# Optimization experiments

Measured on AMD Instinct MI355X. Metric: run time of the kernel, lower is better.

Reference implementation:

```python
import jax, jax.numpy as jnp
from jax import lax
import numpy as np


def conv2d(x, w, pad):
    # x: NCHW, w: OIHW
    return lax.conv_general_dilated(
        x, w, window_strides=(1, 1), padding=[(pad, pad), (pad, pad)],
        dimension_numbers=("NCHW", "OIHW", "NCHW"))


def _scan_dir(x, a, axis, reverse):
    """Directional IRNN scan: cur = relu(x_i + alpha * prev), prev0 = 0.
    a broadcasts as (1, C, 1) over the remaining (B, C, L) slice dims."""
    if reverse:
        x = jnp.flip(x, axis)
    xs = jnp.moveaxis(x, axis, 0)  # (L, B, C, other)

    def step(prev, xi):
        cur = jax.nn.relu(xi + a * prev)
        return cur, cur

    _, hs = lax.scan(step, jnp.zeros_like(xs[0]), xs)
    h = jnp.moveaxis(hs, 0, axis)
    if reverse:
        h = jnp.flip(h, axis)
    return h


def spatial_irnn(x, alpha):
    a = alpha.reshape(1, -1, 1)  # broadcasts over (B, C, W) or (B, C, H)
    h_td = _scan_dir(x, a, axis=2, reverse=False)  # top -> down
    h_dt = _scan_dir(x, a, axis=2, reverse=True)   # down -> top
    h_lr = _scan_dir(x, a, axis=3, reverse=False)  # left -> right
    h_rl = _scan_dir(x, a, axis=3, reverse=True)   # right -> left
    return h_td, h_lr, h_dt, h_rl


def setup_inputs() -> dict:
    key = jax.random.key(0)
    ks = jax.random.split(key, 10)
    B, C, H, W = 8, 32, 256, 256
    mid = C // 2
    s = 0.05
    return {
        "x": jax.random.normal(ks[0], (B, C, H, W), jnp.float32),
        "alpha1": jnp.full((C,), 0.2, jnp.float32),
        "alpha2": jnp.full((C,), 0.2, jnp.float32),
        "w_in": jax.random.normal(ks[1], (C, C, 3, 3), jnp.float32) * s,
        "w2": jax.random.normal(ks[2], (C, 4 * C, 3, 3), jnp.float32) * s,
        "w3": jax.random.normal(ks[3], (C, 4 * C, 3, 3), jnp.float32) * s,
        "att_w1": jax.random.normal(ks[4], (mid, C, 3, 3), jnp.float32) * s,
        "att_w2": jax.random.normal(ks[5], (mid, mid, 3, 3), jnp.float32) * s,
        "att_w3": jax.random.normal(ks[6], (4, mid, 1, 1), jnp.float32) * s,
        "att_b3": jnp.zeros((4,), jnp.float32),
        "w_out": jax.random.normal(ks[7], (1, C, 1, 1), jnp.float32) * s,
    }


def reference(x, alpha1, alpha2, w_in, w2, w3, att_w1, att_w2, att_w3, att_b3, w_out):
    # Attention gate: 4 per-direction weight maps in (0,1)
    a = jax.nn.relu(conv2d(x, att_w1, pad=1))
    a = jax.nn.relu(conv2d(a, att_w2, pad=1))
    weight = jax.nn.sigmoid(conv2d(a, att_w3, pad=0) + att_b3.reshape(1, -1, 1, 1))

    def gate(up, right, down, left):
        return jnp.concatenate([
            up * weight[:, 0:1], right * weight[:, 1:2],
            down * weight[:, 2:3], left * weight[:, 3:4]], axis=1)

    out = conv2d(x, w_in, pad=1)
    up, right, down, left = spatial_irnn(out, alpha1)
    out = conv2d(gate(up, right, down, left), w2, pad=1)
    up, right, down, left = spatial_irnn(out, alpha2)
    out = jax.nn.relu(conv2d(gate(up, right, down, left), w3, pad=1))
    mask = jax.nn.sigmoid(conv2d(out, w_out, pad=0))
    return mask
```

## Files before the change

kernel.cpp:

```cpp
#include <hip/hip_runtime.h>
#include <cstddef>

#define H_ 256
#define W_ 256
#define HW_ 65536

typedef unsigned int uint;
typedef unsigned short ushort;
typedef __attribute__((ext_vector_type(8))) short short8;
typedef __attribute__((ext_vector_type(16))) float floatx16;

__device__ __forceinline__ float bf2f(ushort u) {
    return __uint_as_float(((uint)u) << 16);
}
__device__ __forceinline__ ushort f2bf(float f) {
    uint u = __float_as_uint(f);
    uint r = (u + 0x7fffu + ((u >> 16) & 1u)) >> 16;
    return (ushort)r;
}
__device__ __forceinline__ float sigmoidf_(float x) {
    return 1.0f / (1.0f + expf(-x));
}

__device__ __forceinline__ void prep_one(const float* src, ushort* dst,
                                         int CO, int CI, int e) {
    int chunk = e / 9216;
    int r = e - chunk * 9216;
    int co = r / 288;
    int kk = r - co * 288;
    int khw = kk >> 5;
    int ci = kk & 31;
    int cig = chunk * 32 + ci;
    float v = 0.f;
    if (co < CO && cig < CI) v = src[(co * CI + cig) * 9 + khw];
    int s = kk >> 4;
    int lane = ((kk >> 3) & 1) * 32 + co;
    int j = kk & 7;
    dst[(((size_t)chunk * 18 + s) * 64 + lane) * 8 + j] = f2bf(v);
}

__global__ __launch_bounds__(256) void prep_weights(
    const float* __restrict__ w_in, const float* __restrict__ w2,
    const float* __restrict__ w3, const float* __restrict__ aw1,
    const float* __restrict__ aw2,
    ushort* __restrict__ w_inB, ushort* __restrict__ w2B,
    ushort* __restrict__ w3B, ushort* __restrict__ aw1B,
    ushort* __restrict__ aw2B) {
    int idx = blockIdx.x * 256 + threadIdx.x;
    if (idx < 9216)        prep_one(w_in, w_inB, 32, 32, idx);
    else if (idx < 46080)  prep_one(w2, w2B, 32, 128, idx - 9216);
    else if (idx < 82944)  prep_one(w3, w3B, 32, 128, idx - 46080);
    else if (idx < 92160)  prep_one(aw1, aw1B, 16, 32, idx - 82944);
    else if (idx < 101376) prep_one(aw2, aw2B, 16, 16, idx - 92160);
}

__global__ __launch_bounds__(256) void transform_x(const float* __restrict__ x,
                                                   ushort* __restrict__ xh) {
    __shared__ float s[64][33];
    const int t = threadIdx.x;
    const int w0 = blockIdx.x * 64, h = blockIdx.y, b = blockIdx.z;
    {
        int ww = t & 63, c0 = (t >> 6) * 8;
#pragma unroll
        for (int j = 0; j < 8; j++) {
            int c = c0 + j;
            s[ww][c] = x[((size_t)(b * 32 + c)) * HW_ + h * W_ + w0 + ww];
        }
    }
    __syncthreads();
    {
        int p = t >> 2, cb = t & 3;
        ushort tmp[8];
#pragma unroll
        for (int j = 0; j < 8; j++) tmp[j] = f2bf(s[p][cb * 8 + j]);
        *(uint4*)(xh + (((size_t)b * HW_ + h * W_ + w0 + p) * 32) + cb * 8) =
            *(const uint4*)tmp;
    }
}

template<int NCHUNK, int COOUT, bool RELU>
__global__ __launch_bounds__(256, 4) void conv_mfma(
    const ushort* __restrict__ in0, const ushort* __restrict__ in1,
    const ushort* __restrict__ in2, const ushort* __restrict__ in3,
    const ushort* __restrict__ wB, ushort* __restrict__ outp) {
    __shared__ __align__(16) ushort smem[1360 * 8];
    const int t = threadIdx.x;
    const int wid = t >> 6;
    const int lane = t & 63;
    const int lco = lane & 31, lhalf = lane >> 5;
    const int w0 = blockIdx.x * 32, h0 = blockIdx.y * 8, b = blockIdx.z;
    const ushort* ins[4] = {in0, in1, in2, in3};

    size_t goff[6];
    int slot[6];
    bool ok[6];
#pragma unroll
    for (int i = 0; i < 6; i++) {
        int u = i * 256 + t;
        int row = u / 136;
        int rem = u - row * 136;
        int p = rem >> 2, cb = rem & 3;
        int gh = h0 - 1 + row, gw = w0 - 1 + p;
        ok[i] = (u < 1360) && ((unsigned)gh < 256u) && ((unsigned)gw < 256u);
        goff[i] = ok[i] ? ((((size_t)b * HW_ + (size_t)gh * W_ + gw) * 32) + cb * 8) : 0;
        slot[i] = row * 136 + (p << 2) + (cb ^ (p & 3) ^ ((p >> 2) & 3));
    }

    floatx16 acc0, acc1;
#pragma unroll
    for (int i = 0; i < 16; i++) { acc0[i] = 0.f; acc1[i] = 0.f; }

    for (int ch = 0; ch < NCHUNK; ch++) {
        __syncthreads();
        {
            const ushort* inp = ins[ch];
            uint4 v[6];
#pragma unroll
            for (int i = 0; i < 6; i++) {
                v[i] = make_uint4(0, 0, 0, 0);
                if (ok[i]) v[i] = *(const uint4*)(inp + goff[i]);
            }
#pragma unroll
            for (int i = 0; i < 6; i++) {
                int u = i * 256 + t;
                if (u < 1360) *(uint4*)(smem + (size_t)slot[i] * 8) = v[i];
            }
        }
        __syncthreads();

        const ushort* wbp = wB + ((size_t)ch * 18 * 64 + lane) * 8;
#pragma unroll
        for (int half = 0; half < 2; half++) {
            short8 bf[9];
#pragma unroll
            for (int j = 0; j < 9; j++)
                bf[j] = *(const short8*)(wbp + (size_t)(2 * j + half) * 512);
            const int cbr = half * 2 + lhalf;
#pragma unroll
            for (int kw = 0; kw < 3; kw++) {
                const int ww = lco + kw;
                const int cbs = cbr ^ (ww & 3) ^ ((ww >> 2) & 3);
                short8 a[4];
#pragma unroll
                for (int r = 0; r < 4; r++)
                    a[r] = *(const short8*)(smem + (size_t)((wid * 2 + r) * 136 + (ww << 2) + cbs) * 8);
#pragma unroll
                for (int kh = 0; kh < 3; kh++) {
                    acc0 = __builtin_amdgcn_mfma_f32_32x32x16_bf16(a[kh], bf[kh * 3 + kw], acc0, 0, 0, 0);
                    acc1 = __builtin_amdgcn_mfma_f32_32x32x16_bf16(a[kh + 1], bf[kh * 3 + kw], acc1, 0, 0, 0);
                }
            }
        }
    }

#pragma unroll
    for (int r = 0; r < 16; r++) {
        int prow = (r & 3) + 8 * (r >> 2) + 4 * lhalf;
        float v0 = acc0[r], v1 = acc1[r];
        if (RELU) { v0 = fmaxf(v0, 0.f); v1 = fmaxf(v1, 0.f); }
        ushort u0 = (lco < COOUT) ? f2bf(v0) : (ushort)0;
        ushort u1 = (lco < COOUT) ? f2bf(v1) : (ushort)0;
        size_t p0 = (((size_t)b * HW_ + (h0 + wid * 2) * W_ + w0 + prow) * 32) + lco;
        outp[p0] = u0;
        outp[p0 + (size_t)W_ * 32] = u1;
    }
}

__global__ __launch_bounds__(256) void att1x1(const ushort* __restrict__ a2,
                                              const float* __restrict__ w,
                                              const float* __restrict__ bias,
                                              ushort* __restrict__ wmapT) {
    int idx = blockIdx.x * 256 + threadIdx.x;
    float xin[16];
    {
        uint4 v0 = *(const uint4*)(a2 + (size_t)idx * 32);
        uint4 v1 = *(const uint4*)(a2 + (size_t)idx * 32 + 8);
        const ushort* u = (const ushort*)&v0;
#pragma unroll
        for (int j = 0; j < 8; j++) xin[j] = bf2f(u[j]);
        const ushort* u2 = (const ushort*)&v1;
#pragma unroll
        for (int j = 0; j < 8; j++) xin[8 + j] = bf2f(u2[j]);
    }
#pragma unroll
    for (int g = 0; g < 4; g++) {
        float acc = bias[g];
#pragma unroll
        for (int ci = 0; ci < 16; ci++) acc = fmaf(xin[ci], w[g * 16 + ci], acc);
        wmapT[(size_t)g * 8 * HW_ + idx] = f2bf(sigmoidf_(acc));
    }
}

__global__ __launch_bounds__(256) void out1x1(const ushort* __restrict__ feat,
                                              const float* __restrict__ w,
                                              float* __restrict__ out) {
    int idx = blockIdx.x * 256 + threadIdx.x;
    float acc = 0.f;
    const ushort* f = feat + (size_t)idx * 32;
#pragma unroll
    for (int q = 0; q < 4; q++) {
        uint4 v = *(const uint4*)(f + q * 8);
        const ushort* u = (const ushort*)&v;
#pragma unroll
        for (int j = 0; j < 8; j++) acc = fmaf(bf2f(u[j]), w[q * 8 + j], acc);
    }
    out[idx] = sigmoidf_(acc);
}

template<int VERT>
__global__ __launch_bounds__(256) void scan_seg(
    const ushort* __restrict__ feat, const float* __restrict__ alpha,
    const ushort* __restrict__ wmapT, ushort* __restrict__ gfwd,
    ushort* __restrict__ gbwd, int gf, int gb) {
    const int t = threadIdx.x;
    const int cg = t & 3;
    const int bx = blockIdx.x;
    const int col = (bx & 3) * 64 + (t >> 2);
    const int seg = (bx >> 2) & 7;
    const int dir = (bx >> 5) & 1;
    const int b = bx >> 6;
    const int c0 = cg * 8;

    float a[8];
#pragma unroll
    for (int j = 0; j < 8; j++) a[j] = alpha[c0 + j];

    const ushort* wplane = wmapT + (size_t)(dir ? gb : gf) * 8 * HW_ + (size_t)b * HW_;
    ushort* gout = dir ? gbwd : gfwd;

    const int main0 = seg * 32;
    const int start = (seg == 0) ? 0 : main0 - 16;
    const int cnt = main0 - start + 32;

    auto pixof = [&](int p) -> size_t {
        int phys = dir ? 255 - p : p;
        return VERT ? ((size_t)phys * W_ + col) : ((size_t)col * W_ + phys);
    };

    uint4 xv[4];
    ushort wv[4];
#pragma unroll
    for (int k = 0; k < 4; k++) {
        size_t pix = pixof(start + k);
        xv[k] = *(const uint4*)(feat + ((size_t)b * HW_ + pix) * 32 + c0);
        wv[k] = wplane[pix];
    }
    float prev[8];
#pragma unroll
    for (int j = 0; j < 8; j++) prev[j] = 0.f;

    for (int i = 0; i < cnt; i += 4) {
#pragma unroll
        for (int k = 0; k < 4; k++) {
            const int p = start + i + k;
            uint4 xcur = xv[k];
            ushort wcur = wv[k];
            if (i + k + 4 < cnt) {
                size_t pix = pixof(p + 4);
                xv[k] = *(const uint4*)(feat + ((size_t)b * HW_ + pix) * 32 + c0);
                wv[k] = wplane[pix];
            }
            const ushort* xu = (const ushort*)&xcur;
            if (p >= main0) {
                float wmv = bf2f(wcur);
                ushort o[8];
#pragma unroll
                for (int j = 0; j < 8; j++) {
                    float cur = fmaxf(fmaf(a[j], prev[j], bf2f(xu[j])), 0.f);
                    prev[j] = cur;
                    o[j] = f2bf(cur * wmv);
                }
                *(uint4*)(gout + ((size_t)b * HW_ + pixof(p)) * 32 + c0) = *(const uint4*)o;
            } else {
#pragma unroll
                for (int j = 0; j < 8; j++)
                    prev[j] = fmaxf(fmaf(a[j], prev[j], bf2f(xu[j])), 0.f);
            }
        }
    }
}

extern "C" void kernel_launch(void* const* d_in, const int* in_sizes, int n_in,
                              void* d_out, int out_size, void* d_ws, size_t ws_size,
                              hipStream_t stream) {
    const float* x      = (const float*)d_in[0];
    const float* alpha1 = (const float*)d_in[1];
    const float* alpha2 = (const float*)d_in[2];
    const float* w_in   = (const float*)d_in[3];
    const float* w2     = (const float*)d_in[4];
    const float* w3     = (const float*)d_in[5];
    const float* aw1    = (const float*)d_in[6];
    const float* aw2    = (const float*)d_in[7];
    const float* aw3    = (const float*)d_in[8];
    const float* ab3    = (const float*)d_in[9];
    const float* wout   = (const float*)d_in[10];
    float* out = (float*)d_out;

    const size_t TEN = (size_t)8 * HW_ * 32;
    ushort* p = (ushort*)d_ws;
    ushort* xh    = p; p += TEN;
    ushort* feat  = p; p += TEN;
    ushort* g0    = p; p += TEN;
    ushort* g1    = p; p += TEN;
    ushort* g2    = p; p += TEN;
    ushort* g3    = p; p += TEN;
    ushort* wmapT = p; p += (size_t)4 * 8 * HW_;
    ushort* w_inB = p; p += 9216;
    ushort* w2B   = p; p += 36864;
    ushort* w3B   = p; p += 36864;
    ushort* aw1B  = p; p += 9216;
    ushort* aw2B  = p; p += 9216;

    prep_weights<<<396, 256, 0, stream>>>(w_in, w2, w3, aw1, aw2,
                                          w_inB, w2B, w3B, aw1B, aw2B);
    transform_x<<<dim3(4, 256, 8), 256, 0, stream>>>(x, xh);

    dim3 gconv(8, 32, 8);
    conv_mfma<1, 16, true><<<gconv, 256, 0, stream>>>(xh, xh, xh, xh, aw1B, g0);
    conv_mfma<1, 16, true><<<gconv, 256, 0, stream>>>(g0, g0, g0, g0, aw2B, g1);
    att1x1<<<2048, 256, 0, stream>>>(g1, aw3, ab3, wmapT);

    conv_mfma<1, 32, false><<<gconv, 256, 0, stream>>>(xh, xh, xh, xh, w_inB, feat);

    scan_seg<1><<<512, 256, 0, stream>>>(feat, alpha1, wmapT, g0, g2, 0, 2);
    scan_seg<0><<<512, 256, 0, stream>>>(feat, alpha1, wmapT, g1, g3, 1, 3);

    conv_mfma<4, 32, false><<<gconv, 256, 0, stream>>>(g0, g1, g2, g3, w2B, feat);

    scan_seg<1><<<512, 256, 0, stream>>>(feat, alpha2, wmapT, g0, g2, 0, 2);
    scan_seg<0><<<512, 256, 0, stream>>>(feat, alpha2, wmapT, g1, g3, 1, 3);

    conv_mfma<4, 32, true><<<gconv, 256, 0, stream>>>(g0, g1, g2, g3, w3B, feat);

    out1x1<<<2048, 256, 0, stream>>>(feat, wout, out);
}
```

Baseline: 405.2 us.

## Fuse 1x1 convs into conv epilogues, merge dual convs, prefetch next chunk

The two 1x1 convolutions (attention sigmoid map and output mask) move into the epilogues of the preceding 3x3 MFMA convolutions through a shared-memory transpose, so the separate att1x1 and out1x1 passes and their intermediate tensors are gone. The input conv and the first attention conv share one staged input tile in a new dual kernel. The next input chunk's global loads are issued before the current chunk's MFMAs, and out-of-bounds loads read a zero page instead of branching. Launch bounds drop to 2 waves, and 32-bit offsets replace size_t, which trades occupancy for register headroom.

New measurement: 489.2 us. +20.7%, slower.

```diff
diff --git a/kernel.cpp b/kernel.cpp
--- a/kernel.cpp
+++ b/kernel.cpp
@@ -45,8 +45,9 @@
     const float* __restrict__ aw2,
     ushort* __restrict__ w_inB, ushort* __restrict__ w2B,
     ushort* __restrict__ w3B, ushort* __restrict__ aw1B,
-    ushort* __restrict__ aw2B) {
+    ushort* __restrict__ aw2B, ushort* __restrict__ zp) {
     int idx = blockIdx.x * 256 + threadIdx.x;
+    if (idx < 64) zp[idx] = 0;
     if (idx < 9216)        prep_one(w_in, w_inB, 32, 32, idx);
     else if (idx < 46080)  prep_one(w2, w2B, 32, 128, idx - 9216);
     else if (idx < 82944)  prep_one(w3, w3B, 32, 128, idx - 46080);
@@ -78,11 +79,74 @@
     }
 }
 
-template<int NCHUNK, int COOUT, bool RELU>
-__global__ __launch_bounds__(256, 4) void conv_mfma(
+struct StageDesc {
+    uint goff[6];
+    int slot[6];
+    bool ok[6];
+};
+__device__ __forceinline__ void make_desc(StageDesc& d, int t, int w0, int h0, int b) {
+#pragma unroll
+    for (int i = 0; i < 6; i++) {
+        int u = i * 256 + t;
+        int row = u / 136;
+        int rem = u - row * 136;
+        int p = rem >> 2, cb = rem & 3;
+        int gh = h0 - 1 + row, gw = w0 - 1 + p;
+        d.ok[i] = (u < 1360) && ((unsigned)gh < 256u) && ((unsigned)gw < 256u);
+        d.goff[i] = d.ok[i] ? (((uint)b * HW_ + (uint)gh * W_ + (uint)gw) * 32 + cb * 8) : 0u;
+        d.slot[i] = row * 136 + (p << 2) + (cb ^ (p & 3) ^ ((p >> 2) & 3));
+    }
+}
+__device__ __forceinline__ void gload6(uint4* v, const StageDesc& d,
+                                       const ushort* __restrict__ inp,
+                                       const ushort* __restrict__ zp) {
+#pragma unroll
+    for (int i = 0; i < 6; i++) {
+        const ushort* src = d.ok[i] ? (inp + d.goff[i]) : zp;
+        v[i] = *(const uint4*)src;
+    }
+}
+__device__ __forceinline__ void swrite6(ushort* smem, const uint4* v,
+                                        const StageDesc& d, int t) {
+#pragma unroll
+    for (int i = 0; i < 6; i++) {
+        if (i * 256 + t < 1360) *(uint4*)(smem + (size_t)d.slot[i] * 8) = v[i];
+    }
+}
+__device__ __forceinline__ void mfma_chunk(const ushort* smem, const ushort* wbp,
+                                           int lco, int lhalf, int wid,
+                                           floatx16& acc0, floatx16& acc1) {
+#pragma unroll
+    for (int half = 0; half < 2; half++) {
+        short8 bf[9];
+#pragma unroll
+        for (int j = 0; j < 9; j++)
+            bf[j] = *(const short8*)(wbp + (size_t)(2 * j + half) * 512);
+        const int cbr = half * 2 + lhalf;
+#pragma unroll
+        for (int kw = 0; kw < 3; kw++) {
+            const int ww = lco + kw;
+            const int cbs = cbr ^ (ww & 3) ^ ((ww >> 2) & 3);
+            short8 a[4];
+#pragma unroll
+            for (int r = 0; r < 4; r++)
+                a[r] = *(const short8*)(smem + (size_t)((wid * 2 + r) * 136 + (ww << 2) + cbs) * 8);
+#pragma unroll
+            for (int kh = 0; kh < 3; kh++) {
+                acc0 = __builtin_amdgcn_mfma_f32_32x32x16_bf16(a[kh], bf[kh * 3 + kw], acc0, 0, 0, 0);
+                acc1 = __builtin_amdgcn_mfma_f32_32x32x16_bf16(a[kh + 1], bf[kh * 3 + kw], acc1, 0, 0, 0);
+            }
+        }
+    }
+}
+
+template<int NCHUNK, int EPI, bool RELU>
+__global__ __launch_bounds__(256, 2) void conv_mfma(
     const ushort* __restrict__ in0, const ushort* __restrict__ in1,
     const ushort* __restrict__ in2, const ushort* __restrict__ in3,
-    const ushort* __restrict__ wB, ushort* __restrict__ outp) {
+    const ushort* __restrict__ wB, const ushort* __restrict__ zp,
+    ushort* __restrict__ outp, const float* __restrict__ aux_w,
+    const float* __restrict__ aux_b) {
     __shared__ __align__(16) ushort smem[1360 * 8];
     const int t = threadIdx.x;
     const int wid = t >> 6;
@@ -91,120 +155,114 @@
     const int w0 = blockIdx.x * 32, h0 = blockIdx.y * 8, b = blockIdx.z;
     const ushort* ins[4] = {in0, in1, in2, in3};
 
-    size_t goff[6];
-    int slot[6];
-    bool ok[6];
-#pragma unroll
-    for (int i = 0; i < 6; i++) {
-        int u = i * 256 + t;
-        int row = u / 136;
-        int rem = u - row * 136;
-        int p = rem >> 2, cb = rem & 3;
-        int gh = h0 - 1 + row, gw = w0 - 1 + p;
-        ok[i] = (u < 1360) && ((unsigned)gh < 256u) && ((unsigned)gw < 256u);
-        goff[i] = ok[i] ? ((((size_t)b * HW_ + (size_t)gh * W_ + gw) * 32) + cb * 8) : 0;
-        slot[i] = row * 136 + (p << 2) + (cb ^ (p & 3) ^ ((p >> 2) & 3));
-    }
+    StageDesc d;
+    make_desc(d, t, w0, h0, b);
 
     floatx16 acc0, acc1;
 #pragma unroll
     for (int i = 0; i < 16; i++) { acc0[i] = 0.f; acc1[i] = 0.f; }
 
+    uint4 v[6];
+    gload6(v, d, ins[0], zp);
     for (int ch = 0; ch < NCHUNK; ch++) {
         __syncthreads();
-        {
-            const ushort* inp = ins[ch];
-            uint4 v[6];
-#pragma unroll
-            for (int i = 0; i < 6; i++) {
-                v[i] = make_uint4(0, 0, 0, 0);
-                if (ok[i]) v[i] = *(const uint4*)(inp + goff[i]);
-            }
-#pragma unroll
-            for (int i = 0; i < 6; i++) {
-                int u = i * 256 + t;
-                if (u < 1360) *(uint4*)(smem + (size_t)slot[i] * 8) = v[i];
-            }
-        }
+        swrite6(smem, v, d, t);
         __syncthreads();
-
-        const ushort* wbp = wB + ((size_t)ch * 18 * 64 + lane) * 8;
-#pragma unroll
-        for (int half = 0; half < 2; half++) {
-            short8 bf[9];
-#pragma unroll
-            for (int j = 0; j < 9; j++)
-                bf[j] = *(const short8*)(wbp + (size_t)(2 * j + half) * 512);
-            const int cbr = half * 2 + lhalf;
-#pragma unroll
-            for (int kw = 0; kw < 3; kw++) {
-                const int ww = lco + kw;
-                const int cbs = cbr ^ (ww & 3) ^ ((ww >> 2) & 3);
-                short8 a[4];
-#pragma unroll
-                for (int r = 0; r < 4; r++)
-                    a[r] = *(const short8*)(smem + (size_t)((wid * 2 + r) * 136 + (ww << 2) + cbs) * 8);
-#pragma unroll
-                for (int kh = 0; kh < 3; kh++) {
-                    acc0 = __builtin_amdgcn_mfma_f32_32x32x16_bf16(a[kh], bf[kh * 3 + kw], acc0, 0, 0, 0);
-                    acc1 = __builtin_amdgcn_mfma_f32_32x32x16_bf16(a[kh + 1], bf[kh * 3 + kw], acc1, 0, 0, 0);
-                }
-            }
-        }
-    }
+        if (ch + 1 < NCHUNK) gload6(v, d, ins[ch + 1], zp);
+        mfma_chunk(smem, wB + ((size_t)ch * 18 * 64 + lane) * 8, lco, lhalf, wid,
+                   acc0, acc1);
+    }
+
+    if (EPI == 0) {
+#pragma unroll
+        for (int r = 0; r < 16; r++) {
+            int wl = (r & 3) + 8 * (r >> 2) + 4 * lhalf;
+            float v0 = acc0[r], v1 = acc1[r];
+            if (RELU) { v0 = fmaxf(v0, 0.f); v1 = fmaxf(v1, 0.f); }
+            size_t p0 = (((size_t)b * HW_ + (h0 + wid * 2) * W_ + w0 + wl) * 32) + lco;
+            outp[p0] = f2bf(v0);
+            outp[p0 + (size_t)W_ * 32] = f2bf(v1);
+        }
+    } else {
+        __syncthreads();
+#pragma unroll
+        for (int r = 0; r < 16; r++) {
+            int wl = (r & 3) + 8 * (r >> 2) + 4 * lhalf;
+            float v0 = acc0[r], v1 = acc1[r];
+            if (RELU) { v0 = fmaxf(v0, 0.f); v1 = fmaxf(v1, 0.f); }
+            int pix0 = (wid * 2) * 32 + wl;
+            smem[(size_t)pix0 * 40 + lco] = f2bf(v0);
+            smem[(size_t)(pix0 + 32) * 40 + lco] = f2bf(v1);
+        }
+        __syncthreads();
+        const int wl = t & 31, hl = t >> 5;
+        const ushort* tp = smem + (size_t)t * 40;
+        if (EPI == 1) {
+            float xin[16];
+            uint4 q0 = *(const uint4*)tp;
+            uint4 q1 = *(const uint4*)(tp + 8);
+            const ushort* u0 = (const ushort*)&q0;
+            const ushort* u1 = (const ushort*)&q1;
+#pragma unroll
+            for (int j = 0; j < 8; j++) { xin[j] = bf2f(u0[j]); xin[8 + j] = bf2f(u1[j]); }
+            size_t pix = (size_t)b * HW_ + (size_t)(h0 + hl) * W_ + w0 + wl;
+#pragma unroll
+            for (int g = 0; g < 4; g++) {
+                float acc = aux_b[g];
+#pragma unroll
+                for (int ci = 0; ci < 16; ci++) acc = fmaf(xin[ci], aux_w[g * 16 + ci], acc);
+                outp[(size_t)g * 8 * HW_ + pix] = f2bf(sigmoidf_(acc));
+            }
+        } else {
+            float acc = 0.f;
+#pragma unroll
+            for (int q = 0; q < 4; q++) {
+                uint4 qv = *(const uint4*)(tp + q * 8);
+                const ushort* uq = (const ushort*)&qv;
+#pragma unroll
+                for (int j = 0; j < 8; j++) acc = fmaf(bf2f(uq[j]), aux_w[q * 8 + j], acc);
+            }
+            float* fo = (float*)outp;
+            fo[(size_t)b * HW_ + (size_t)(h0 + hl) * W_ + w0 + wl] = sigmoidf_(acc);
+        }
+    }
+}
+
+__global__ __launch_bounds__(256, 2) void conv_dual(
+    const ushort* __restrict__ in0, const ushort* __restrict__ wBa,
+    const ushort* __restrict__ wBb, const ushort* __restrict__ zp,
+    ushort* __restrict__ outA, ushort* __restrict__ outB) {
+    __shared__ __align__(16) ushort smem[1360 * 8];
+    const int t = threadIdx.x;
+    const int wid = t >> 6;
+    const int lane = t & 63;
+    const int lco = lane & 31, lhalf = lane >> 5;
+    const int w0 = blockIdx.x * 32, h0 = blockIdx.y * 8, b = blockIdx.z;
+
+    StageDesc d;
+    make_desc(d, t, w0, h0, b);
+
+    floatx16 accA0, accA1, accB0, accB1;
+#pragma unroll
+    for (int i = 0; i < 16; i++) { accA0[i] = 0.f; accA1[i] = 0.f; accB0[i] = 0.f; accB1[i] = 0.f; }
+
+    uint4 v[6];
+    gload6(v, d, in0, zp);
+    __syncthreads();
+    swrite6(smem, v, d, t);
+    __syncthreads();
+    mfma_chunk(smem, wBa + (size_t)lane * 8, lco, lhalf, wid, accA0, accA1);
+    mfma_chunk(smem, wBb + (size_t)lane * 8, lco, lhalf, wid, accB0, accB1);
 
 #pragma unroll
     for (int r = 0; r < 16; r++) {
-        int prow = (r & 3) + 8 * (r >> 2) + 4 * lhalf;
-        float v0 = acc0[r], v1 = acc1[r];
-        if (RELU) { v0 = fmaxf(v0, 0.f); v1 = fmaxf(v1, 0.f); }
-        ushort u0 = (lco < COOUT) ? f2bf(v0) : (ushort)0;
-        ushort u1 = (lco < COOUT) ? f2bf(v1) : (ushort)0;
-        size_t p0 = (((size_t)b * HW_ + (h0 + wid * 2) * W_ + w0 + prow) * 32) + lco;
-        outp[p0] = u0;
-        outp[p0 + (size_t)W_ * 32] = u1;
-    }
-}
-
-__global__ __launch_bounds__(256) void att1x1(const ushort* __restrict__ a2,
-                                              const float* __restrict__ w,
-                                              const float* __restrict__ bias,
-                                              ushort* __restrict__ wmapT) {
-    int idx = blockIdx.x * 256 + threadIdx.x;
-    float xin[16];
-    {
-        uint4 v0 = *(const uint4*)(a2 + (size_t)idx * 32);
-        uint4 v1 = *(const uint4*)(a2 + (size_t)idx * 32 + 8);
-        const ushort* u = (const ushort*)&v0;
-#pragma unroll
-        for (int j = 0; j < 8; j++) xin[j] = bf2f(u[j]);
-        const ushort* u2 = (const ushort*)&v1;
-#pragma unroll
-        for (int j = 0; j < 8; j++) xin[8 + j] = bf2f(u2[j]);
-    }
-#pragma unroll
-    for (int g = 0; g < 4; g++) {
-        float acc = bias[g];
-#pragma unroll
-        for (int ci = 0; ci < 16; ci++) acc = fmaf(xin[ci], w[g * 16 + ci], acc);
-        wmapT[(size_t)g * 8 * HW_ + idx] = f2bf(sigmoidf_(acc));
-    }
-}
-
-__global__ __launch_bounds__(256) void out1x1(const ushort* __restrict__ feat,
-                                              const float* __restrict__ w,
-                                              float* __restrict__ out) {
-    int idx = blockIdx.x * 256 + threadIdx.x;
-    float acc = 0.f;
-    const ushort* f = feat + (size_t)idx * 32;
-#pragma unroll
-    for (int q = 0; q < 4; q++) {
-        uint4 v = *(const uint4*)(f + q * 8);
-        const ushort* u = (const ushort*)&v;
-#pragma unroll
-        for (int j = 0; j < 8; j++) acc = fmaf(bf2f(u[j]), w[q * 8 + j], acc);
-    }
-    out[idx] = sigmoidf_(acc);
+        int wl = (r & 3) + 8 * (r >> 2) + 4 * lhalf;
+        size_t p0 = (((size_t)b * HW_ + (h0 + wid * 2) * W_ + w0 + wl) * 32) + lco;
+        outA[p0] = f2bf(accA0[r]);
+        outA[p0 + (size_t)W_ * 32] = f2bf(accA1[r]);
+        outB[p0] = f2bf(fmaxf(accB0[r], 0.f));
+        outB[p0 + (size_t)W_ * 32] = f2bf(fmaxf(accB1[r], 0.f));
+    }
 }
 
 template<int VERT>
@@ -310,27 +368,28 @@
     ushort* w3B   = p; p += 36864;
     ushort* aw1B  = p; p += 9216;
     ushort* aw2B  = p; p += 9216;
+    ushort* zp    = p; p += 64;
+    ushort* a1z   = g1;
 
     prep_weights<<<396, 256, 0, stream>>>(w_in, w2, w3, aw1, aw2,
-                                          w_inB, w2B, w3B, aw1B, aw2B);
+                                          w_inB, w2B, w3B, aw1B, aw2B, zp);
     transform_x<<<dim3(4, 256, 8), 256, 0, stream>>>(x, xh);
 
     dim3 gconv(8, 32, 8);
-    conv_mfma<1, 16, true><<<gconv, 256, 0, stream>>>(xh, xh, xh, xh, aw1B, g0);
-    conv_mfma<1, 16, true><<<gconv, 256, 0, stream>>>(g0, g0, g0, g0, aw2B, g1);
-    att1x1<<<2048, 256, 0, stream>>>(g1, aw3, ab3, wmapT);
-
-    conv_mfma<1, 32, false><<<gconv, 256, 0, stream>>>(xh, xh, xh, xh, w_inB, feat);
+
+    conv_dual<<<gconv, 256, 0, stream>>>(xh, w_inB, aw1B, zp, feat, a1z);
+    conv_mfma<1, 1, true><<<gconv, 256, 0, stream>>>(a1z, a1z, a1z, a1z, aw2B, zp,
+                                                     wmapT, aw3, ab3);
 
     scan_seg<1><<<512, 256, 0, stream>>>(feat, alpha1, wmapT, g0, g2, 0, 2);
     scan_seg<0><<<512, 256, 0, stream>>>(feat, alpha1, wmapT, g1, g3, 1, 3);
 
-    conv_mfma<4, 32, false><<<gconv, 256, 0, stream>>>(g0, g1, g2, g3, w2B, feat);
+    conv_mfma<4, 0, false><<<gconv, 256, 0, stream>>>(g0, g1, g2, g3, w2B, zp,
+                                                      feat, nullptr, nullptr);
 
     scan_seg<1><<<512, 256, 0, stream>>>(feat, alpha2, wmapT, g0, g2, 0, 2);
     scan_seg<0><<<512, 256, 0, stream>>>(feat, alpha2, wmapT, g1, g3, 1, 3);
 
-    conv_mfma<4, 32, true><<<gconv, 256, 0, stream>>>(g0, g1, g2, g3, w3B, feat);
-
-    out1x1<<<2048, 256, 0, stream>>>(feat, wout, out);
-}
+    conv_mfma<4, 2, true><<<gconv, 256, 0, stream>>>(g0, g1, g2, g3, w3B, zp,
+                                                     (ushort*)out, wout, nullptr);
+}
```
